# Optimization experiments

Hardware: AMD Instinct MI355X
Metric: run time of the kernel (lower is better)

The kernel has to match this reference:

```python
import jax, jax.numpy as jnp
import numpy as np

EMBED_DIM = 512
NUM_HEAD = 16
HEAD_DIM = EMBED_DIM // NUM_HEAD
EPS = 1e-6


def setup_inputs() -> dict:
    key = jax.random.key(0)
    ks = jax.random.split(key, 7)
    B, L = 4, 4096
    scale = 1.0 / np.sqrt(EMBED_DIM)
    return {
        "query": jax.random.normal(ks[0], (B, L, EMBED_DIM), jnp.float32),
        "key": jax.random.normal(ks[1], (B, L, EMBED_DIM), jnp.float32),
        "value": jax.random.normal(ks[2], (B, L, EMBED_DIM), jnp.float32),
        "Wq": jax.random.normal(ks[3], (EMBED_DIM, EMBED_DIM), jnp.float32) * scale,
        "Wk": jax.random.normal(ks[4], (EMBED_DIM, EMBED_DIM), jnp.float32) * scale,
        "Wv": jax.random.normal(ks[5], (EMBED_DIM, EMBED_DIM), jnp.float32) * scale,
        "Wm": jax.random.normal(ks[6], (EMBED_DIM, EMBED_DIM), jnp.float32) * scale,
    }


def reference(query, key, value, Wq, Wk, Wv, Wm):
    bs, Lq, E = query.shape
    H, D = NUM_HEAD, HEAD_DIM
    # projections (nn.Linear without bias: x @ W.T)
    q = (query @ Wq.T).reshape(bs, Lq, H, D)
    k = (key @ Wk.T).reshape(bs, -1, H, D)
    v = (value @ Wv.T).reshape(bs, -1, H, D)
    # elu+1 feature map
    Q = jax.nn.elu(q) + 1.0
    K = jax.nn.elu(k) + 1.0
    v_len = v.shape[1]
    v = v / v_len
    # KV accumulation: [n, h, d, dv]
    KV = jnp.einsum('nshd,nshv->nhdv', K, v)
    # normalizer Z: [n, l, h]
    Z = 1.0 / (jnp.einsum('nlhd,nhd->nlh', Q, K.sum(axis=1)) + EPS)
    # weighted combination: [n, l, h, dv]
    message = jnp.einsum('nlhd,nhdv,nlh->nlhv', Q, KV, Z) * v_len
    # merge projection (dropout p=0 -> identity)
    out = message.reshape(bs, Lq, H * D) @ Wm.T
    return out
```

## Files before the change

kernel.cpp:

```cpp
#include <hip/hip_runtime.h>

#define EMBED  512
#define NHEAD  16
#define HDIM   32
#define NBATCH 4
#define SEQ    4096
#define NROWS  (NBATCH * SEQ)
#define NE     (NROWS * EMBED)
#define WN     (EMBED * EMBED)
#define FEPS   1e-6f

typedef __attribute__((ext_vector_type(8))) short short8;
typedef __attribute__((ext_vector_type(4))) float f32x4;

__device__ __forceinline__ short f2bf(float x) {
    unsigned u = __float_as_uint(x);
    u += 0x7FFFu + ((u >> 16) & 1u);
    return (short)(u >> 16);
}
__device__ __forceinline__ float bf2f(short h) {
    return __uint_as_float(((unsigned)(unsigned short)h) << 16);
}

#define GLDS16(gp, lp)                                                   \
    __builtin_amdgcn_global_load_lds(                                    \
        (__attribute__((address_space(1))) void*)(void*)(gp),            \
        (__attribute__((address_space(3))) void*)(void*)(lp), 16, 0, 0)

__global__ __launch_bounds__(256)
void convert_all(const float* __restrict__ q, const float* __restrict__ k,
                 const float* __restrict__ v,
                 const float* __restrict__ wq, const float* __restrict__ wk,
                 const float* __restrict__ wv, const float* __restrict__ wm,
                 short* __restrict__ qh, short* __restrict__ ql,
                 short* __restrict__ kh, short* __restrict__ kl,
                 short* __restrict__ vh, short* __restrict__ vl,
                 short* __restrict__ wqh, short* __restrict__ wql,
                 short* __restrict__ wkh, short* __restrict__ wkl,
                 short* __restrict__ wvh, short* __restrict__ wvl,
                 short* __restrict__ wmh, short* __restrict__ wml) {
    const int b = blockIdx.x;
    const float* src; short* dh; short* dl; int boff;
    if (b < 12288) {
        const int s = b >> 12;
        src = (s == 0) ? q  : (s == 1) ? k  : v;
        dh  = (s == 0) ? qh : (s == 1) ? kh : vh;
        dl  = (s == 0) ? ql : (s == 1) ? kl : vl;
        boff = b & 4095;
    } else {
        const int s = (b - 12288) >> 7;
        src = (s == 0) ? wq  : (s == 1) ? wk  : (s == 2) ? wv  : wm;
        dh  = (s == 0) ? wqh : (s == 1) ? wkh : (s == 2) ? wvh : wmh;
        dl  = (s == 0) ? wql : (s == 1) ? wkl : (s == 2) ? wvl : wml;
        boff = (b - 12288) & 127;
    }
    const size_t i = ((size_t)boff * 256 + threadIdx.x) * 8;
    float4 x0 = *(const float4*)(src + i);
    float4 x1 = *(const float4*)(src + i + 4);
    float vv[8] = {x0.x, x0.y, x0.z, x0.w, x1.x, x1.y, x1.z, x1.w};
    short8 h, l;
#pragma unroll
    for (int t = 0; t < 8; ++t) {
        short hb = f2bf(vv[t]);
        h[t] = hb;
        l[t] = f2bf(vv[t] - bf2f(hb));
    }
    *(short8*)(dh + i) = h;
    *(short8*)(dl + i) = l;
}

__global__ __launch_bounds__(256, 3)
void qkv_gemm(const short* __restrict__ Aqh, const short* __restrict__ Aql,
              const short* __restrict__ Akh, const short* __restrict__ Akl,
              const short* __restrict__ Avh, const short* __restrict__ Avl,
              const short* __restrict__ WqH, const short* __restrict__ WqL,
              const short* __restrict__ WkH, const short* __restrict__ WkL,
              const short* __restrict__ WvH, const short* __restrict__ WvL,
              float* __restrict__ Qb, float* __restrict__ Kb,
              float* __restrict__ Vb) {
    __shared__ short lds[4][128][32];

    const int tid  = threadIdx.x;
    const int lane = tid & 63;
    const int wave = tid >> 6;
    const int wm   = (wave >> 1) * 64;
    const int wn   = (wave & 1) * 64;
    const int l15  = lane & 15;
    const int kg   = lane >> 4;

    const int lin = blockIdx.x;
    const int op  = lin >> 9;
    const int r_  = lin & 511;
    const int bn  = (r_ >> 7) * 128;
    const int bm  = (r_ & 127) * 128;

    const short* Ah = (op == 0) ? Aqh : (op == 1) ? Akh : Avh;
    const short* Al = (op == 0) ? Aql : (op == 1) ? Akl : Avl;
    const short* Bh = (op == 0) ? WqH : (op == 1) ? WkH : WvH;
    const short* Bl = (op == 0) ? WqL : (op == 1) ? WkL : WvL;
    float* C = (op == 0) ? Qb : (op == 1) ? Kb : Vb;

    const int sr = lane >> 2;
    const int sc = (((lane & 3) ^ ((lane >> 3) & 3)) << 3);
    const int rt = wave * 32 + sr;
    const short* gAh = Ah + (size_t)(bm + rt) * EMBED + sc;
    const short* gAl = Al + (size_t)(bm + rt) * EMBED + sc;
    const short* gBh = Bh + (size_t)(bn + rt) * EMBED + sc;
    const short* gBl = Bl + (size_t)(bn + rt) * EMBED + sc;

    short* dAh = &lds[0][wave * 32][0];
    short* dAl = &lds[1][wave * 32][0];
    short* dBh = &lds[2][wave * 32][0];
    short* dBl = &lds[3][wave * 32][0];

    const int rk = ((kg ^ ((l15 >> 1) & 3)) << 3);

    f32x4 acc[4][4];
#pragma unroll
    for (int i = 0; i < 4; ++i)
#pragma unroll
        for (int j = 0; j < 4; ++j) acc[i][j] = (f32x4)0.0f;

#pragma unroll 1
    for (int k0 = 0; k0 < EMBED; k0 += 32) {
        GLDS16(gAh + k0,              dAh);
        GLDS16(gAh + 16 * EMBED + k0, dAh + 512);
        GLDS16(gAl + k0,              dAl);
        GLDS16(gAl + 16 * EMBED + k0, dAl + 512);
        GLDS16(gBh + k0,              dBh);
        GLDS16(gBh + 16 * EMBED + k0, dBh + 512);
        GLDS16(gBl + k0,              dBl);
        GLDS16(gBl + 16 * EMBED + k0, dBl + 512);
        __syncthreads();

        short8 ahv[4], alv[4], bhv[4], blv[4];
#pragma unroll
        for (int i = 0; i < 4; ++i) {
            ahv[i] = *(const short8*)&lds[0][wm + i * 16 + l15][rk];
            alv[i] = *(const short8*)&lds[1][wm + i * 16 + l15][rk];
            bhv[i] = *(const short8*)&lds[2][wn + i * 16 + l15][rk];
            blv[i] = *(const short8*)&lds[3][wn + i * 16 + l15][rk];
        }
#pragma unroll
        for (int i = 0; i < 4; ++i)
#pragma unroll
            for (int j = 0; j < 4; ++j) {
                acc[i][j] = __builtin_amdgcn_mfma_f32_16x16x32_bf16(ahv[i], bhv[j], acc[i][j], 0, 0, 0);
                acc[i][j] = __builtin_amdgcn_mfma_f32_16x16x32_bf16(ahv[i], blv[j], acc[i][j], 0, 0, 0);
                acc[i][j] = __builtin_amdgcn_mfma_f32_16x16x32_bf16(alv[i], bhv[j], acc[i][j], 0, 0, 0);
            }
        __syncthreads();
    }

#pragma unroll
    for (int i = 0; i < 4; ++i)
#pragma unroll
        for (int j = 0; j < 4; ++j) {
            const int col = bn + wn + j * 16 + l15;
#pragma unroll
            for (int r = 0; r < 4; ++r) {
                const int row = bm + wm + i * 16 + kg * 4 + r;
                float vv = acc[i][j][r];
                if (op < 2) vv = (vv > 0.f) ? (vv + 1.f) : __expf(vv);
                else        vv = vv * (1.0f / (float)SEQ);
                C[(size_t)row * EMBED + col] = vv;
            }
        }
}

__global__ __launch_bounds__(256, 3)
void merge_gemm(const short* __restrict__ Mh, const short* __restrict__ Ml,
                const short* __restrict__ WhP, const short* __restrict__ WlP,
                float* __restrict__ C) {
    __shared__ short lds[4][128][32];

    const int tid  = threadIdx.x;
    const int lane = tid & 63;
    const int wave = tid >> 6;
    const int wm   = (wave >> 1) * 64;
    const int wn   = (wave & 1) * 64;
    const int l15  = lane & 15;
    const int kg   = lane >> 4;

    const int lin = blockIdx.x;
    const int bn  = (lin >> 7) * 128;
    const int bm  = (lin & 127) * 128;

    const int sr = lane >> 2;
    const int sc = (((lane & 3) ^ ((lane >> 3) & 3)) << 3);
    const int rt = wave * 32 + sr;
    const short* gAh = Mh  + (size_t)(bm + rt) * EMBED + sc;
    const short* gAl = Ml  + (size_t)(bm + rt) * EMBED + sc;
    const short* gBh = WhP + (size_t)(bn + rt) * EMBED + sc;
    const short* gBl = WlP + (size_t)(bn + rt) * EMBED + sc;

    short* dAh = &lds[0][wave * 32][0];
    short* dAl = &lds[1][wave * 32][0];
    short* dBh = &lds[2][wave * 32][0];
    short* dBl = &lds[3][wave * 32][0];

    const int rk = ((kg ^ ((l15 >> 1) & 3)) << 3);

    f32x4 acc[4][4];
#pragma unroll
    for (int i = 0; i < 4; ++i)
#pragma unroll
        for (int j = 0; j < 4; ++j) acc[i][j] = (f32x4)0.0f;

#pragma unroll 1
    for (int k0 = 0; k0 < EMBED; k0 += 32) {
        GLDS16(gAh + k0,              dAh);
        GLDS16(gAh + 16 * EMBED + k0, dAh + 512);
        GLDS16(gAl + k0,              dAl);
        GLDS16(gAl + 16 * EMBED + k0, dAl + 512);
        GLDS16(gBh + k0,              dBh);
        GLDS16(gBh + 16 * EMBED + k0, dBh + 512);
        GLDS16(gBl + k0,              dBl);
        GLDS16(gBl + 16 * EMBED + k0, dBl + 512);
        __syncthreads();

        short8 ahv[4], alv[4], bhv[4], blv[4];
#pragma unroll
        for (int i = 0; i < 4; ++i) {
            ahv[i] = *(const short8*)&lds[0][wm + i * 16 + l15][rk];
            alv[i] = *(const short8*)&lds[1][wm + i * 16 + l15][rk];
            bhv[i] = *(const short8*)&lds[2][wn + i * 16 + l15][rk];
            blv[i] = *(const short8*)&lds[3][wn + i * 16 + l15][rk];
        }
#pragma unroll
        for (int i = 0; i < 4; ++i)
#pragma unroll
            for (int j = 0; j < 4; ++j) {
                acc[i][j] = __builtin_amdgcn_mfma_f32_16x16x32_bf16(ahv[i], bhv[j], acc[i][j], 0, 0, 0);
                acc[i][j] = __builtin_amdgcn_mfma_f32_16x16x32_bf16(ahv[i], blv[j], acc[i][j], 0, 0, 0);
                acc[i][j] = __builtin_amdgcn_mfma_f32_16x16x32_bf16(alv[i], bhv[j], acc[i][j], 0, 0, 0);
            }
        __syncthreads();
    }

#pragma unroll
    for (int i = 0; i < 4; ++i)
#pragma unroll
        for (int j = 0; j < 4; ++j) {
            const int col = bn + wn + j * 16 + l15;
#pragma unroll
            for (int r = 0; r < 4; ++r) {
                const int row = bm + wm + i * 16 + kg * 4 + r;
                C[(size_t)row * EMBED + col] = acc[i][j][r];
            }
        }
}

__global__ __launch_bounds__(256)
void kv_ksum_mfma(const float* __restrict__ Kf, const float* __restrict__ Vf,
                  float* __restrict__ KV, float* __restrict__ Ksum) {
    __shared__ char smem[34816];
    short (*Kh)[34] = (short (*)[34])smem;
    short (*Kl)[34] = (short (*)[34])(smem + 8704);
    short (*Vh)[34] = (short (*)[34])(smem + 17408);
    short (*Vl)[34] = (short (*)[34])(smem + 26112);

    const int bh_ = blockIdx.y;
    const int b = bh_ >> 4, h = bh_ & 15;
    const int s0 = blockIdx.x * 256;
    const int t = threadIdx.x;
    const int lane = t & 63, wave = t >> 6;
    const int l15 = lane & 15, kg = lane >> 4;
    const int ws = wave * 32;

    const int sl = t >> 1;
    const int dsel = (t & 1) * 16;
    const float* Kbase = Kf + (size_t)b * SEQ * EMBED + h * HDIM;
    const float* Vbase = Vf + (size_t)b * SEQ * EMBED + h * HDIM;

    f32x4 kvacc[2][2], ksacc[2];
#pragma unroll
    for (int i = 0; i < 2; ++i) {
        ksacc[i] = (f32x4)0.0f;
#pragma unroll
        for (int j = 0; j < 2; ++j) kvacc[i][j] = (f32x4)0.0f;
    }
    short8 ones;
#pragma unroll
    for (int q = 0; q < 8; ++q) ones[q] = (short)0x3F80;

    float4 kx[4], vx[4];
#pragma unroll
    for (int p = 0; p < 4; ++p) {
        kx[p] = *(const float4*)(Kbase + (size_t)(s0 + sl) * EMBED + dsel + 4 * p);
        vx[p] = *(const float4*)(Vbase + (size_t)(s0 + sl) * EMBED + dsel + 4 * p);
    }

#pragma unroll 1
    for (int it = 0; it < 2; ++it) {
        __syncthreads();
        {
            float kv_[8] = {kx[0].x, kx[0].y, kx[0].z, kx[0].w, kx[1].x, kx[1].y, kx[1].z, kx[1].w};
            float kv2[8] = {kx[2].x, kx[2].y, kx[2].z, kx[2].w, kx[3].x, kx[3].y, kx[3].z, kx[3].w};
            float vv_[8] = {vx[0].x, vx[0].y, vx[0].z, vx[0].w, vx[1].x, vx[1].y, vx[1].z, vx[1].w};
            float vv2[8] = {vx[2].x, vx[2].y, vx[2].z, vx[2].w, vx[3].x, vx[3].y, vx[3].z, vx[3].w};
            short8 h0, l0, h1, l1;
#pragma unroll
            for (int q = 0; q < 8; ++q) { short hb = f2bf(kv_[q]); h0[q] = hb; l0[q] = f2bf(kv_[q] - bf2f(hb)); }
#pragma unroll
            for (int q = 0; q < 8; ++q) { short hb = f2bf(kv2[q]); h1[q] = hb; l1[q] = f2bf(kv2[q] - bf2f(hb)); }
            *(short8*)&Kh[sl][dsel] = h0; *(short8*)&Kh[sl][dsel + 8] = h1;
            *(short8*)&Kl[sl][dsel] = l0; *(short8*)&Kl[sl][dsel + 8] = l1;
#pragma unroll
            for (int q = 0; q < 8; ++q) { short hb = f2bf(vv_[q]); h0[q] = hb; l0[q] = f2bf(vv_[q] - bf2f(hb)); }
#pragma unroll
            for (int q = 0; q < 8; ++q) { short hb = f2bf(vv2[q]); h1[q] = hb; l1[q] = f2bf(vv2[q] - bf2f(hb)); }
            *(short8*)&Vh[sl][dsel] = h0; *(short8*)&Vh[sl][dsel + 8] = h1;
            *(short8*)&Vl[sl][dsel] = l0; *(short8*)&Vl[sl][dsel + 8] = l1;
        }
        __syncthreads();
        if (it == 0) {
#pragma unroll
            for (int p = 0; p < 4; ++p) {
                kx[p] = *(const float4*)(Kbase + (size_t)(s0 + 128 + sl) * EMBED + dsel + 4 * p);
                vx[p] = *(const float4*)(Vbase + (size_t)(s0 + 128 + sl) * EMBED + dsel + 4 * p);
            }
        }
        short8 kah[2], kal[2], vbh[2], vbl[2];
#pragma unroll
        for (int i = 0; i < 2; ++i) {
#pragma unroll
            for (int q = 0; q < 8; ++q) {
                const int srow = ws + kg * 8 + q;
                const int col  = i * 16 + l15;
                kah[i][q] = Kh[srow][col];
                kal[i][q] = Kl[srow][col];
                vbh[i][q] = Vh[srow][col];
                vbl[i][q] = Vl[srow][col];
            }
        }
#pragma unroll
        for (int i = 0; i < 2; ++i) {
#pragma unroll
            for (int j = 0; j < 2; ++j) {
                kvacc[i][j] = __builtin_amdgcn_mfma_f32_16x16x32_bf16(kah[i], vbh[j], kvacc[i][j], 0, 0, 0);
                kvacc[i][j] = __builtin_amdgcn_mfma_f32_16x16x32_bf16(kah[i], vbl[j], kvacc[i][j], 0, 0, 0);
                kvacc[i][j] = __builtin_amdgcn_mfma_f32_16x16x32_bf16(kal[i], vbh[j], kvacc[i][j], 0, 0, 0);
            }
            ksacc[i] = __builtin_amdgcn_mfma_f32_16x16x32_bf16(kah[i], ones, ksacc[i], 0, 0, 0);
            ksacc[i] = __builtin_amdgcn_mfma_f32_16x16x32_bf16(kal[i], ones, ksacc[i], 0, 0, 0);
        }
    }

    __syncthreads();
    float* red = (float*)smem;
    float* myred = red + wave * 1056;
#pragma unroll
    for (int i = 0; i < 2; ++i)
#pragma unroll
        for (int j = 0; j < 2; ++j)
#pragma unroll
            for (int r = 0; r < 4; ++r)
                myred[(i * 16 + kg * 4 + r) * 32 + j * 16 + l15] = kvacc[i][j][r];
    if (l15 == 0) {
#pragma unroll
        for (int i = 0; i < 2; ++i)
#pragma unroll
            for (int r = 0; r < 4; ++r)
                myred[1024 + i * 16 + kg * 4 + r] = ksacc[i][r];
    }
    __syncthreads();
    float* kvout = KV + (size_t)bh_ * 1024;
    for (int idx = t; idx < 1024; idx += 256) {
        float s4 = red[idx] + red[1056 + idx] + red[2112 + idx] + red[3168 + idx];
        atomicAdd(&kvout[idx], s4);
    }
    if (t < 32) {
        float s4 = red[1024 + t] + red[1056 + 1024 + t] + red[2112 + 1024 + t] + red[3168 + 1024 + t];
        atomicAdd(&Ksum[bh_ * 32 + t], s4);
    }
}

__global__ __launch_bounds__(512)
void message_kernel(const float* __restrict__ Q, const float* __restrict__ KV,
                    const float* __restrict__ Ksum,
                    short* __restrict__ Mh, short* __restrict__ Ml) {
    const int blk  = blockIdx.x;
    const int row0 = blk * 4;
    const int b    = row0 >> 12;
    const int t    = threadIdx.x;
    const int h    = t >> 5, e = t & 31;

    __shared__ float q[4][EMBED];
    __shared__ float ks[EMBED];
    ks[t] = Ksum[b * EMBED + t];
#pragma unroll
    for (int r = 0; r < 4; ++r) q[r][t] = Q[(size_t)(row0 + r) * EMBED + t];

    const float* kvh = KV + (size_t)(b * NHEAD + h) * HDIM * HDIM + e;
    float kc[HDIM];
#pragma unroll
    for (int d = 0; d < HDIM; ++d) kc[d] = kvh[d * HDIM];
    __syncthreads();

#pragma unroll
    for (int r = 0; r < 4; ++r) {
        float zden = FEPS, m = 0.f;
#pragma unroll
        for (int d = 0; d < HDIM; ++d) {
            float qd = q[r][h * HDIM + d];
            zden = fmaf(qd, ks[h * HDIM + d], zden);
            m    = fmaf(qd, kc[d], m);
        }
        float vv = m * ((float)SEQ / zden);
        short hb = f2bf(vv);
        Mh[(size_t)(row0 + r) * EMBED + t] = hb;
        Ml[(size_t)(row0 + r) * EMBED + t] = f2bf(vv - bf2f(hb));
    }
}

extern "C" void kernel_launch(void* const* d_in, const int* in_sizes, int n_in,
                              void* d_out, int out_size, void* d_ws, size_t ws_size,
                              hipStream_t stream) {
    const float* query = (const float*)d_in[0];
    const float* key   = (const float*)d_in[1];
    const float* value = (const float*)d_in[2];
    const float* Wq    = (const float*)d_in[3];
    const float* Wk    = (const float*)d_in[4];
    const float* Wv    = (const float*)d_in[5];
    const float* Wm    = (const float*)d_in[6];
    float* out = (float*)d_out;

    float* ws  = (float*)d_ws;
    float* Qb  = ws;
    float* Kb  = Qb + (size_t)NE;
    float* Vb  = Kb + (size_t)NE;
    float* KVb = Vb + (size_t)NE;
    float* KSb = KVb + 64 * 1024;
    short* wsp = (short*)(KSb + 64 * HDIM);
    short* WqH = wsp;            short* WqL = wsp + WN;
    short* WkH = wsp + 2 * WN;   short* WkL = wsp + 3 * WN;
    short* WvH = wsp + 4 * WN;   short* WvL = wsp + 5 * WN;
    short* WmH = wsp + 6 * WN;   short* WmL = wsp + 7 * WN;
    short* Xp  = wsp + 8 * WN;
    short* Qih = Xp;             short* Qil = Xp + (size_t)NE;
    short* Kih = Xp + 2 * (size_t)NE;  short* Kil = Xp + 3 * (size_t)NE;
    short* Vih = Xp + 4 * (size_t)NE;  short* Vil = Xp + 5 * (size_t)NE;
    short* Mh = (short*)Kb;
    short* Ml = Mh + (size_t)NE;

    hipMemsetAsync(KVb, 0, (64 * 1024 + 64 * HDIM) * sizeof(float), stream);

    convert_all<<<12800, 256, 0, stream>>>(query, key, value, Wq, Wk, Wv, Wm,
                                           Qih, Qil, Kih, Kil, Vih, Vil,
                                           WqH, WqL, WkH, WkL,
                                           WvH, WvL, WmH, WmL);

    qkv_gemm<<<1536, 256, 0, stream>>>(Qih, Qil, Kih, Kil, Vih, Vil,
                                       WqH, WqL, WkH, WkL, WvH, WvL,
                                       Qb, Kb, Vb);

    kv_ksum_mfma<<<dim3(16, 64), 256, 0, stream>>>(Kb, Vb, KVb, KSb);
    message_kernel<<<NROWS / 4, 512, 0, stream>>>(Qb, KVb, KSb, Mh, Ml);

    merge_gemm<<<512, 256, 0, stream>>>(Mh, Ml, WmH, WmL, out);
}
```

Before: 306.9 us.

## Triple-buffer LDS pipeline in split-bf16 GEMMs with larger 256x128 tiles

Factors the QKV and merge GEMMs into a shared core that uses 512-thread blocks with 256x128 output tiles. Global-to-LDS loads run two stages ahead through a three-slot LDS ring, gated by vmcnt waits and a single barrier per k-step, and MFMA issue priority is raised during compute. The aim is to hide global load latency and halve the per-tile barrier count, with better B-tile reuse. In exchange it uses more LDS per block (three 48 KB slots) and has fewer blocks in flight, and correctness depends on hand-tuned waitcnt counts.

```diff
diff --git a/kernel.cpp b/kernel.cpp
--- a/kernel.cpp
+++ b/kernel.cpp
@@ -69,7 +69,83 @@
     *(short8*)(dl + i) = l;
 }
 
-__global__ __launch_bounds__(256, 3)
+__device__ __forceinline__ void gemm_core(
+    const short* __restrict__ Ahp, const short* __restrict__ Alp,
+    const short* __restrict__ Bhp, const short* __restrict__ Blp,
+    int bmG, int bnG, short (*lds)[24576], f32x4 acc[4][4])
+{
+    const int tid  = threadIdx.x;
+    const int lane = tid & 63;
+    const int wave = tid >> 6;
+    const int l15  = lane & 15;
+    const int kg   = lane >> 4;
+
+    const int sc8 = (((lane & 3) ^ ((lane >> 3) & 3)) << 3);
+    const size_t aR0 = (size_t)(bmG + wave * 32 + (lane >> 2)) * EMBED + sc8;
+    const size_t bR0 = (size_t)(bnG + wave * 16 + (lane >> 2)) * EMBED + sc8;
+
+    const int dA = wave * 1024;
+    const int dB = wave * 512;
+
+    const int rk8   = ((kg ^ ((l15 >> 1) & 3)) << 3);
+    const int aBase = ((wave >> 1) * 64 + l15) * 32 + rk8;
+    const int bBase = 16384 + ((wave & 1) * 64 + l15) * 32 + rk8;
+
+#pragma unroll
+    for (int v = 0; v < 2; ++v) {
+        short* T = lds[v];
+        const int kp = v * 32;
+        GLDS16(Ahp + aR0 + kp,              T + dA);
+        GLDS16(Ahp + aR0 + 16 * EMBED + kp, T + dA + 512);
+        GLDS16(Alp + aR0 + kp,              T + 8192 + dA);
+        GLDS16(Alp + aR0 + 16 * EMBED + kp, T + 8192 + dA + 512);
+        GLDS16(Bhp + bR0 + kp,              T + 16384 + dB);
+        GLDS16(Blp + bR0 + kp,              T + 20480 + dB);
+    }
+
+    int rs = 0;
+#pragma unroll 1
+    for (int s = 0; s < 16; ++s) {
+        if (s < 15) asm volatile("s_waitcnt vmcnt(6)" ::: "memory");
+        else        asm volatile("s_waitcnt vmcnt(0)" ::: "memory");
+        __builtin_amdgcn_s_barrier();
+        __builtin_amdgcn_sched_barrier(0);
+
+        short* S = lds[rs];
+        short8 fah[4], fal[4], fbh[4], fbl[4];
+#pragma unroll
+        for (int f = 0; f < 4; ++f) {
+            fah[f] = *(const short8*)(S + aBase + f * 512);
+            fal[f] = *(const short8*)(S + 8192 + aBase + f * 512);
+            fbh[f] = *(const short8*)(S + bBase + f * 512);
+            fbl[f] = *(const short8*)(S + 4096 + bBase + f * 512);
+        }
+        if (s < 14) {
+            const int ws2 = (rs + 2 >= 3) ? (rs - 1) : (rs + 2);
+            short* T = lds[ws2];
+            const int kp = (s + 2) * 32;
+            GLDS16(Ahp + aR0 + kp,              T + dA);
+            GLDS16(Ahp + aR0 + 16 * EMBED + kp, T + dA + 512);
+            GLDS16(Alp + aR0 + kp,              T + 8192 + dA);
+            GLDS16(Alp + aR0 + 16 * EMBED + kp, T + 8192 + dA + 512);
+            GLDS16(Bhp + bR0 + kp,              T + 16384 + dB);
+            GLDS16(Blp + bR0 + kp,              T + 20480 + dB);
+        }
+        __builtin_amdgcn_s_setprio(1);
+#pragma unroll
+        for (int i = 0; i < 4; ++i)
+#pragma unroll
+            for (int j = 0; j < 4; ++j) {
+                acc[i][j] = __builtin_amdgcn_mfma_f32_16x16x32_bf16(fah[i], fbh[j], acc[i][j], 0, 0, 0);
+                acc[i][j] = __builtin_amdgcn_mfma_f32_16x16x32_bf16(fah[i], fbl[j], acc[i][j], 0, 0, 0);
+                acc[i][j] = __builtin_amdgcn_mfma_f32_16x16x32_bf16(fal[i], fbh[j], acc[i][j], 0, 0, 0);
+            }
+        __builtin_amdgcn_s_setprio(0);
+        rs = (rs == 2) ? 0 : rs + 1;
+    }
+}
+
+__global__ __launch_bounds__(512, 2)
 void qkv_gemm(const short* __restrict__ Aqh, const short* __restrict__ Aql,
               const short* __restrict__ Akh, const short* __restrict__ Akl,
               const short* __restrict__ Avh, const short* __restrict__ Avl,
@@ -78,21 +154,13 @@
               const short* __restrict__ WvH, const short* __restrict__ WvL,
               float* __restrict__ Qb, float* __restrict__ Kb,
               float* __restrict__ Vb) {
-    __shared__ short lds[4][128][32];
-
-    const int tid  = threadIdx.x;
-    const int lane = tid & 63;
-    const int wave = tid >> 6;
-    const int wm   = (wave >> 1) * 64;
-    const int wn   = (wave & 1) * 64;
-    const int l15  = lane & 15;
-    const int kg   = lane >> 4;
+    __shared__ short lds[3][24576];
 
     const int lin = blockIdx.x;
-    const int op  = lin >> 9;
-    const int r_  = lin & 511;
-    const int bn  = (r_ >> 7) * 128;
-    const int bm  = (r_ & 127) * 128;
+    const int op  = lin >> 8;
+    const int r_  = lin & 255;
+    const int bnG = ((r_ >> 6) & 3) * 128;
+    const int bmG = (r_ & 63) * 256;
 
     const short* Ah = (op == 0) ? Aqh : (op == 1) ? Akh : Avh;
     const short* Al = (op == 0) ? Aql : (op == 1) ? Akl : Avl;
@@ -100,66 +168,28 @@
     const short* Bl = (op == 0) ? WqL : (op == 1) ? WkL : WvL;
     float* C = (op == 0) ? Qb : (op == 1) ? Kb : Vb;
 
-    const int sr = lane >> 2;
-    const int sc = (((lane & 3) ^ ((lane >> 3) & 3)) << 3);
-    const int rt = wave * 32 + sr;
-    const short* gAh = Ah + (size_t)(bm + rt) * EMBED + sc;
-    const short* gAl = Al + (size_t)(bm + rt) * EMBED + sc;
-    const short* gBh = Bh + (size_t)(bn + rt) * EMBED + sc;
-    const short* gBl = Bl + (size_t)(bn + rt) * EMBED + sc;
-
-    short* dAh = &lds[0][wave * 32][0];
-    short* dAl = &lds[1][wave * 32][0];
-    short* dBh = &lds[2][wave * 32][0];
-    short* dBl = &lds[3][wave * 32][0];
-
-    const int rk = ((kg ^ ((l15 >> 1) & 3)) << 3);
-
     f32x4 acc[4][4];
 #pragma unroll
     for (int i = 0; i < 4; ++i)
 #pragma unroll
         for (int j = 0; j < 4; ++j) acc[i][j] = (f32x4)0.0f;
 
-#pragma unroll 1
-    for (int k0 = 0; k0 < EMBED; k0 += 32) {
-        GLDS16(gAh + k0,              dAh);
-        GLDS16(gAh + 16 * EMBED + k0, dAh + 512);
-        GLDS16(gAl + k0,              dAl);
-        GLDS16(gAl + 16 * EMBED + k0, dAl + 512);
-        GLDS16(gBh + k0,              dBh);
-        GLDS16(gBh + 16 * EMBED + k0, dBh + 512);
-        GLDS16(gBl + k0,              dBl);
-        GLDS16(gBl + 16 * EMBED + k0, dBl + 512);
-        __syncthreads();
-
-        short8 ahv[4], alv[4], bhv[4], blv[4];
-#pragma unroll
-        for (int i = 0; i < 4; ++i) {
-            ahv[i] = *(const short8*)&lds[0][wm + i * 16 + l15][rk];
-            alv[i] = *(const short8*)&lds[1][wm + i * 16 + l15][rk];
-            bhv[i] = *(const short8*)&lds[2][wn + i * 16 + l15][rk];
-            blv[i] = *(const short8*)&lds[3][wn + i * 16 + l15][rk];
-        }
-#pragma unroll
-        for (int i = 0; i < 4; ++i)
-#pragma unroll
-            for (int j = 0; j < 4; ++j) {
-                acc[i][j] = __builtin_amdgcn_mfma_f32_16x16x32_bf16(ahv[i], bhv[j], acc[i][j], 0, 0, 0);
-                acc[i][j] = __builtin_amdgcn_mfma_f32_16x16x32_bf16(ahv[i], blv[j], acc[i][j], 0, 0, 0);
-                acc[i][j] = __builtin_amdgcn_mfma_f32_16x16x32_bf16(alv[i], bhv[j], acc[i][j], 0, 0, 0);
-            }
-        __syncthreads();
-    }
-
+    gemm_core(Ah, Al, Bh, Bl, bmG, bnG, lds, acc);
+
+    const int lane = threadIdx.x & 63;
+    const int wave = threadIdx.x >> 6;
+    const int l15  = lane & 15;
+    const int kg   = lane >> 4;
+    const int wm   = (wave >> 1) * 64;
+    const int wn   = (wave & 1) * 64;
 #pragma unroll
     for (int i = 0; i < 4; ++i)
 #pragma unroll
         for (int j = 0; j < 4; ++j) {
-            const int col = bn + wn + j * 16 + l15;
+            const int col = bnG + wn + j * 16 + l15;
 #pragma unroll
             for (int r = 0; r < 4; ++r) {
-                const int row = bm + wm + i * 16 + kg * 4 + r;
+                const int row = bmG + wm + i * 16 + kg * 4 + r;
                 float vv = acc[i][j][r];
                 if (op < 2) vv = (vv > 0.f) ? (vv + 1.f) : __expf(vv);
                 else        vv = vv * (1.0f / (float)SEQ);
@@ -168,84 +198,38 @@
         }
 }
 
-__global__ __launch_bounds__(256, 3)
+__global__ __launch_bounds__(512, 2)
 void merge_gemm(const short* __restrict__ Mh, const short* __restrict__ Ml,
                 const short* __restrict__ WhP, const short* __restrict__ WlP,
                 float* __restrict__ C) {
-    __shared__ short lds[4][128][32];
-
-    const int tid  = threadIdx.x;
-    const int lane = tid & 63;
-    const int wave = tid >> 6;
+    __shared__ short lds[3][24576];
+
+    const int lin = blockIdx.x;
+    const int bnG = ((lin >> 6) & 3) * 128;
+    const int bmG = (lin & 63) * 256;
+
+    f32x4 acc[4][4];
+#pragma unroll
+    for (int i = 0; i < 4; ++i)
+#pragma unroll
+        for (int j = 0; j < 4; ++j) acc[i][j] = (f32x4)0.0f;
+
+    gemm_core(Mh, Ml, WhP, WlP, bmG, bnG, lds, acc);
+
+    const int lane = threadIdx.x & 63;
+    const int wave = threadIdx.x >> 6;
+    const int l15  = lane & 15;
+    const int kg   = lane >> 4;
     const int wm   = (wave >> 1) * 64;
     const int wn   = (wave & 1) * 64;
-    const int l15  = lane & 15;
-    const int kg   = lane >> 4;
-
-    const int lin = blockIdx.x;
-    const int bn  = (lin >> 7) * 128;
-    const int bm  = (lin & 127) * 128;
-
-    const int sr = lane >> 2;
-    const int sc = (((lane & 3) ^ ((lane >> 3) & 3)) << 3);
-    const int rt = wave * 32 + sr;
-    const short* gAh = Mh  + (size_t)(bm + rt) * EMBED + sc;
-    const short* gAl = Ml  + (size_t)(bm + rt) * EMBED + sc;
-    const short* gBh = WhP + (size_t)(bn + rt) * EMBED + sc;
-    const short* gBl = WlP + (size_t)(bn + rt) * EMBED + sc;
-
-    short* dAh = &lds[0][wave * 32][0];
-    short* dAl = &lds[1][wave * 32][0];
-    short* dBh = &lds[2][wave * 32][0];
-    short* dBl = &lds[3][wave * 32][0];
-
-    const int rk = ((kg ^ ((l15 >> 1) & 3)) << 3);
-
-    f32x4 acc[4][4];
 #pragma unroll
     for (int i = 0; i < 4; ++i)
 #pragma unroll
-        for (int j = 0; j < 4; ++j) acc[i][j] = (f32x4)0.0f;
-
-#pragma unroll 1
-    for (int k0 = 0; k0 < EMBED; k0 += 32) {
-        GLDS16(gAh + k0,              dAh);
-        GLDS16(gAh + 16 * EMBED + k0, dAh + 512);
-        GLDS16(gAl + k0,              dAl);
-        GLDS16(gAl + 16 * EMBED + k0, dAl + 512);
-        GLDS16(gBh + k0,              dBh);
-        GLDS16(gBh + 16 * EMBED + k0, dBh + 512);
-        GLDS16(gBl + k0,              dBl);
-        GLDS16(gBl + 16 * EMBED + k0, dBl + 512);
-        __syncthreads();
-
-        short8 ahv[4], alv[4], bhv[4], blv[4];
-#pragma unroll
-        for (int i = 0; i < 4; ++i) {
-            ahv[i] = *(const short8*)&lds[0][wm + i * 16 + l15][rk];
-            alv[i] = *(const short8*)&lds[1][wm + i * 16 + l15][rk];
-            bhv[i] = *(const short8*)&lds[2][wn + i * 16 + l15][rk];
-            blv[i] = *(const short8*)&lds[3][wn + i * 16 + l15][rk];
-        }
-#pragma unroll
-        for (int i = 0; i < 4; ++i)
-#pragma unroll
-            for (int j = 0; j < 4; ++j) {
-                acc[i][j] = __builtin_amdgcn_mfma_f32_16x16x32_bf16(ahv[i], bhv[j], acc[i][j], 0, 0, 0);
-                acc[i][j] = __builtin_amdgcn_mfma_f32_16x16x32_bf16(ahv[i], blv[j], acc[i][j], 0, 0, 0);
-                acc[i][j] = __builtin_amdgcn_mfma_f32_16x16x32_bf16(alv[i], bhv[j], acc[i][j], 0, 0, 0);
-            }
-        __syncthreads();
-    }
-
-#pragma unroll
-    for (int i = 0; i < 4; ++i)
-#pragma unroll
         for (int j = 0; j < 4; ++j) {
-            const int col = bn + wn + j * 16 + l15;
+            const int col = bnG + wn + j * 16 + l15;
 #pragma unroll
             for (int r = 0; r < 4; ++r) {
-                const int row = bm + wm + i * 16 + kg * 4 + r;
+                const int row = bmG + wm + i * 16 + kg * 4 + r;
                 C[(size_t)row * EMBED + col] = acc[i][j][r];
             }
         }
@@ -451,12 +435,12 @@
                                            WqH, WqL, WkH, WkL,
                                            WvH, WvL, WmH, WmL);
 
-    qkv_gemm<<<1536, 256, 0, stream>>>(Qih, Qil, Kih, Kil, Vih, Vil,
-                                       WqH, WqL, WkH, WkL, WvH, WvL,
-                                       Qb, Kb, Vb);
+    qkv_gemm<<<768, 512, 0, stream>>>(Qih, Qil, Kih, Kil, Vih, Vil,
+                                      WqH, WqL, WkH, WkL, WvH, WvL,
+                                      Qb, Kb, Vb);
 
     kv_ksum_mfma<<<dim3(16, 64), 256, 0, stream>>>(Kb, Vb, KVb, KSb);
     message_kernel<<<NROWS / 4, 512, 0, stream>>>(Qb, KVb, KSb, Mh, Ml);
 
-    merge_gemm<<<512, 256, 0, stream>>>(Mh, Ml, WmH, WmL, out);
-}
+    merge_gemm<<<256, 512, 0, stream>>>(Mh, Ml, WmH, WmL, out);
+}
```

Measured after the change: 303.1 us. About the same (-1.2%).
